# Optimization experiments

Measured on AMD Instinct MI355X. Metric: run time of the kernel, lower is better.

Reference implementation:

```python
import math
import jax, jax.numpy as jnp
import numpy as np

B, L, D, H, FF = 32, 796, 512, 8, 2048
HD = D // H          # 64
CS, STRIDE = 16, 13  # clip_size=16, overlap_area_size=3 -> stride 13
NC = (L - CS) // STRIDE + 1  # 61 clips, tiles L exactly


def _ln(v):
    m = jnp.mean(v, axis=-1, keepdims=True)
    s = jnp.mean((v - m) ** 2, axis=-1, keepdims=True)
    return (v - m) / jnp.sqrt(s + 1e-6)


def setup_inputs() -> dict:
    key = jax.random.key(0)
    ks = iter(jax.random.split(key, 64))
    def w(*shape):
        return jax.random.normal(next(ks), shape, jnp.float32) * 0.02
    inp = {
        "x": jax.random.normal(next(ks), (B, L, D), jnp.float32),
        "mask": jnp.ones((B, 1, L), dtype=bool),
        # global block params
        "g_ln_g": jnp.ones((D,), jnp.float32), "g_ln_b": jnp.zeros((D,), jnp.float32),
        "Wq": w(D, D), "Wk": w(D, D), "Wv": w(D, D), "Wo": w(D, D),
        "bq": jnp.zeros((D,), jnp.float32), "bk": jnp.zeros((D,), jnp.float32),
        "bv": jnp.zeros((D,), jnp.float32), "bo": jnp.zeros((D,), jnp.float32),
        "f_ln_g": jnp.ones((D,), jnp.float32), "f_ln_b": jnp.zeros((D,), jnp.float32),
        "W1": w(D, FF), "b1": jnp.zeros((FF,), jnp.float32),
        "W2": w(FF, D), "b2": jnp.zeros((D,), jnp.float32),
        # per-batch-element clip params (ModuleList of 32 -> stacked leading dim B)
        "c_ln_g": jnp.ones((B, D), jnp.float32), "c_ln_b": jnp.zeros((B, D), jnp.float32),
        "cWq": w(B, D, D), "cWk": w(B, D, D), "cWv": w(B, D, D), "cWo": w(B, D, D),
        "cbq": jnp.zeros((B, D), jnp.float32), "cbk": jnp.zeros((B, D), jnp.float32),
        "cbv": jnp.zeros((B, D), jnp.float32), "cbo": jnp.zeros((B, D), jnp.float32),
        "cf_ln_g": jnp.ones((B, D), jnp.float32), "cf_ln_b": jnp.zeros((B, D), jnp.float32),
        "cW1": w(B, D, FF), "cb1": jnp.zeros((B, FF), jnp.float32),
        "cW2": w(B, FF, D), "cb2": jnp.zeros((B, D), jnp.float32),
    }
    return inp


def reference(x, mask, g_ln_g, g_ln_b, Wq, Wk, Wv, Wo, bq, bk, bv, bo,
              f_ln_g, f_ln_b, W1, b1, W2, b2,
              c_ln_g, c_ln_b, cWq, cWk, cWv, cWo, cbq, cbk, cbv, cbo,
              cf_ln_g, cf_ln_b, cW1, cb1, cW2, cb2):
    # ---- clip partition: overlapping length-16 windows, stride 13 ----
    starts = np.arange(NC) * STRIDE
    idx = starts[:, None] + np.arange(CS)            # [NC, CS]
    clips = x[:, idx]                                 # [B, NC, CS, D]
    cmask = mask[:, 0][:, idx]                        # [B, NC, CS]
    # channel shuffle on last 384 dims: view(nc,16,24,16).permute(0,3,2,1)
    c1 = clips[..., :128]
    c2 = clips[..., 128:].reshape(B, NC, CS, 24, 16)
    c2 = jnp.transpose(c2, (0, 1, 4, 3, 2)).reshape(B, NC, CS, 384)
    clips = jnp.concatenate([c1, c2], axis=-1)        # [B, NC, CS, D]
    # ---- per-batch-element clip LN + MHA + FFN (distinct weights per b) ----
    cn = _ln(clips) * c_ln_g[:, None, None, :] + c_ln_b[:, None, None, :]
    q = (jnp.einsum('bncd,bde->bnce', cn, cWq) + cbq[:, None, None, :]).reshape(B, NC, CS, H, HD)
    k = (jnp.einsum('bncd,bde->bnce', cn, cWk) + cbk[:, None, None, :]).reshape(B, NC, CS, H, HD)
    v = (jnp.einsum('bncd,bde->bnce', cn, cWv) + cbv[:, None, None, :]).reshape(B, NC, CS, H, HD)
    q = q / math.sqrt(HD)
    sc = jnp.einsum('bnqhd,bnkhd->bnhqk', q, k)       # [B, NC, H, CS, CS]
    sc = jnp.where(cmask[:, :, None, None, :], sc, -jnp.inf)
    a = jax.nn.softmax(sc, axis=-1)
    ctx = jnp.einsum('bnhqk,bnkhd->bnqhd', a, v).reshape(B, NC, CS, D)
    mh = jnp.einsum('bncd,bde->bnce', ctx, cWo) + cbo[:, None, None, :]
    hcl = mh + clips                                  # dropout = identity (eval)
    fn = _ln(hcl) * cf_ln_g[:, None, None, :] + cf_ln_b[:, None, None, :]
    fmid = jax.nn.relu(jnp.einsum('bncd,bdf->bncf', fn, cW1) + cb1[:, None, None, :])
    clips_out = jnp.einsum('bncf,bfd->bncd', fmid, cW2) + cb2[:, None, None, :] + hcl
    p = np.arange(L)
    cidx = np.minimum(p // STRIDE, NC - 1)
    off = p - cidx * STRIDE
    x_rec = clips_out[:, cidx, off]                   # [B, L, D]
    # ---- global LN + MHA + residual + FFN ----
    xn = _ln(x_rec) * g_ln_g + g_ln_b
    q2 = (xn @ Wq + bq).reshape(B, L, H, HD) / math.sqrt(HD)
    k2 = (xn @ Wk + bk).reshape(B, L, H, HD)
    v2 = (xn @ Wv + bv).reshape(B, L, H, HD)
    sc2 = jnp.einsum('bqhd,bkhd->bhqk', q2, k2)
    sc2 = jnp.where(mask[:, None, :, :], sc2, -jnp.inf)
    ctx2 = jnp.einsum('bhqk,bkhd->bqhd', jax.nn.softmax(sc2, axis=-1), v2).reshape(B, L, D)
    h = ctx2 @ Wo + bo + x
    hn = _ln(h) * f_ln_g + f_ln_b
    o = jax.nn.relu(hn @ W1 + b1) @ W2 + b2 + h
    return o
```

## Files before the change

### kernel.cpp

```cpp
#include <hip/hip_runtime.h>

#define B_   32
#define L_   796
#define D_   512
#define H_   8
#define HD_  64
#define FF_  2048
#define CS_  16
#define STR_ 13
#define NC_  61
#define NQT_ 13
#define NQT2_ 7
#define MC_  976
#define QKVS 1536
#define QS   (0.125f * 1.44269504f)

typedef __attribute__((ext_vector_type(8))) short short8;
typedef __attribute__((ext_vector_type(4))) short short4v;
typedef __attribute__((ext_vector_type(4))) float f32x4;

__device__ __forceinline__ unsigned short f2bf(float x) {
    unsigned u = __float_as_uint(x);
    unsigned r = u + 0x7FFFu + ((u >> 16) & 1u);
    return (unsigned short)(r >> 16);
}
__device__ __forceinline__ float bf2f(unsigned short h) {
    return __uint_as_float(((unsigned)h) << 16);
}
__device__ __forceinline__ float ex2(float x) {
    return __builtin_amdgcn_exp2f(x);
}
__device__ __forceinline__ void gload16(const unsigned short* g, unsigned short* l) {
    __builtin_amdgcn_global_load_lds(
        (const __attribute__((address_space(1))) void*)g,
        (__attribute__((address_space(3))) void*)l, 16, 0, 0);
}

__global__ __launch_bounds__(256) void k_ln(const float* __restrict__ in,
                                            unsigned short* __restrict__ out,
                                            const float* __restrict__ gamma,
                                            const float* __restrict__ beta,
                                            int rows_per_batch, int gstride, int gather)
{
    __shared__ float red[8];
    long long row = blockIdx.x;
    int tid = threadIdx.x;
    int b;
    float v0, v1;
    if (gather == 2) {
        b = (int)(row / MC_);
        int rr = (int)(row % MC_);
        int n = rr >> 4, c = rr & 15;
        long long xb = (long long)b * L_ * D_;
        int d0 = tid, st0, sd0;
        if (d0 < 128) { st0 = n * STR_ + c; sd0 = d0; }
        else { int j = d0 - 128; st0 = n * STR_ + (j & 15); sd0 = 128 + ((j >> 4) << 4) + c; }
        v0 = in[xb + (long long)st0 * D_ + sd0];
        int j1 = tid + 128;
        int st1 = n * STR_ + (j1 & 15), sd1 = 128 + ((j1 >> 4) << 4) + c;
        v1 = in[xb + (long long)st1 * D_ + sd1];
    } else {
        long long srow = row;
        if (gather == 1) {
            int p = (int)(row % L_);
            b = (int)(row / L_);
            int ci = p / STR_; if (ci > NC_ - 1) ci = NC_ - 1;
            srow = ((long long)b * NC_ + ci) * CS_ + (p - ci * STR_);
        } else {
            b = (int)(row / rows_per_batch);
        }
        const float* xr = in + srow * D_;
        v0 = xr[tid]; v1 = xr[tid + 256];
    }
    float s = v0 + v1;
#pragma unroll
    for (int off = 1; off < 64; off <<= 1) s += __shfl_xor(s, off);
    if ((tid & 63) == 0) red[tid >> 6] = s;
    __syncthreads();
    float mean = (red[0] + red[1] + red[2] + red[3]) * (1.0f / 512.0f);
    float d0 = v0 - mean, d1 = v1 - mean;
    float vv = d0 * d0 + d1 * d1;
#pragma unroll
    for (int off = 1; off < 64; off <<= 1) vv += __shfl_xor(vv, off);
    if ((tid & 63) == 0) red[4 + (tid >> 6)] = vv;
    __syncthreads();
    float var = (red[4] + red[5] + red[6] + red[7]) * (1.0f / 512.0f);
    float rstd = rsqrtf(var + 1e-6f);
    const float* g  = gamma + (long long)b * gstride;
    const float* bt = beta  + (long long)b * gstride;
    unsigned short* o = out + row * D_;
    o[tid]       = f2bf(d0 * rstd * g[tid]       + bt[tid]);
    o[tid + 256] = f2bf(d1 * rstd * g[tid + 256] + bt[tid + 256]);
}

__global__ __launch_bounds__(256) void k_wt(const float* __restrict__ W,
                                            unsigned short* __restrict__ T,
                                            int rowStride, int tStride,
                                            long long sWb, long long sTb)
{
    __shared__ float t[32][33];
    int z = blockIdx.z;
    const float* Wz = W + (long long)z * sWb;
    unsigned short* Tz = T + (long long)z * sTb;
    int n0 = blockIdx.x << 5, k0 = blockIdx.y << 5;
    int tx = threadIdx.x & 31, ty = threadIdx.x >> 5;
#pragma unroll
    for (int i = 0; i < 4; i++) {
        int k = ty + (i << 3);
        t[k][tx] = Wz[(long long)(k0 + k) * rowStride + n0 + tx];
    }
    __syncthreads();
#pragma unroll
    for (int i = 0; i < 4; i++) {
        int n = ty + (i << 3);
        Tz[(long long)(n0 + n) * tStride + k0 + tx] = f2bf(t[tx][n]);
    }
}

__global__ __launch_bounds__(256) void k_wt_stack(const float* __restrict__ Wa,
                                                  const float* __restrict__ Wb,
                                                  const float* __restrict__ Wc,
                                                  const float* __restrict__ Wd,
                                                  unsigned short* __restrict__ T,
                                                  int nb, int ntens, long long sWb)
{
    __shared__ float t[32][33];
    int z = blockIdx.z;
    int tt = z / nb, b = z % nb;
    const float* Wz = (tt == 0 ? Wa : tt == 1 ? Wb : tt == 2 ? Wc : Wd)
                      + (long long)b * sWb;
    unsigned short* Tz = T + ((long long)b * ntens + tt) * (512 * 512);
    int n0 = blockIdx.x << 5, k0 = blockIdx.y << 5;
    int tx = threadIdx.x & 31, ty = threadIdx.x >> 5;
#pragma unroll
    for (int i = 0; i < 4; i++) {
        int k = ty + (i << 3);
        t[k][tx] = Wz[(long long)(k0 + k) * 512 + n0 + tx];
    }
    __syncthreads();
#pragma unroll
    for (int i = 0; i < 4; i++) {
        int n = ty + (i << 3);
        Tz[(long long)(n0 + n) * 512 + k0 + tx] = f2bf(t[tx][n]);
    }
}

__global__ __launch_bounds__(512) void k_gemm_mfma(
    const unsigned short* __restrict__ A, const unsigned short* __restrict__ WT,
    const float* __restrict__ b0p, const float* __restrict__ b1p,
    const float* __restrict__ b2p,
    const float* res, const float* __restrict__ xg, void* Cout,
    int M, int N, int K, int ldwk, int NX, int NYd, int mode,
    long long sAb, long long sWb, long long sBb, long long sRb, long long sCb,
    float alpha, float alpha1, int relu, int biasmode, int resmode, int outbf16)
{
    __shared__ unsigned short lds[16384];
    int tid = threadIdx.x;

    int bid = blockIdx.x;
    int xcd = bid & 7, inner = bid >> 3;
    int x = inner % NX, t = inner / NX;
    int y, z;
    if (mode == 0) { y = t % NYd; z = (t / NYd) * 8 + xcd; }
    else           { y = t * 8 + xcd; z = 0; }
    int row0 = y << 7, col0 = x << 7;
    if (row0 >= M) return;

    const unsigned short* Ab = A + z * sAb;
    const unsigned short* Wb = WT + z * sWb;

    int w = tid >> 6, lane = tid & 63;
    int wr = (w >> 2) << 6;
    int wc = (w & 3) << 5;
    int l15 = lane & 15, lg = lane >> 4;
    int lrow4 = lane >> 2, lslot = lane & 3;

    f32x4 acc[4][2];
#pragma unroll
    for (int i = 0; i < 4; i++)
#pragma unroll
        for (int j = 0; j < 2; j++) acc[i][j] = (f32x4)0.f;

    const int nt = K >> 5;
    int srow = (w << 4) + lrow4;
    int skey = (srow >> 1) & 3;

#pragma unroll
    for (int pt = 0; pt < 2; ++pt) {
        int k0 = pt << 5;
        unsigned short* sA = lds + (pt << 13);
        unsigned short* sW = sA + 4096;
        gload16(Ab + (long long)(row0 + srow) * K + k0 + ((lslot ^ skey) << 3),
                sA + ((w << 4) << 5));
        gload16(Wb + (long long)(col0 + srow) * ldwk + k0 + ((lslot ^ skey) << 3),
                sW + ((w << 4) << 5));
    }

    for (int kt = 0; kt < nt; ++kt) {
        if (kt + 1 < nt) asm volatile("s_waitcnt vmcnt(2)" ::: "memory");
        else             asm volatile("s_waitcnt vmcnt(0)" ::: "memory");
        __builtin_amdgcn_s_barrier();

        unsigned short* lA = lds + ((kt & 1) << 13);
        unsigned short* lW = lA + 4096;

        short8 af[4], bfr[2];
#pragma unroll
        for (int mf = 0; mf < 4; mf++) {
            int r = wr + (mf << 4) + l15;
            af[mf] = *(const short8*)(lA + (r << 5) + ((lg ^ ((r >> 1) & 3)) << 3));
        }
#pragma unroll
        for (int nf = 0; nf < 2; nf++) {
            int r = wc + (nf << 4) + l15;
            bfr[nf] = *(const short8*)(lW + (r << 5) + ((lg ^ ((r >> 1) & 3)) << 3));
        }

        asm volatile("s_waitcnt lgkmcnt(0)" ::: "memory");
        __builtin_amdgcn_s_barrier();

        if (kt + 2 < nt) {
            int k0 = (kt + 2) << 5;
            gload16(Ab + (long long)(row0 + srow) * K + k0 + ((lslot ^ skey) << 3),
                    lA + ((w << 4) << 5));
            gload16(Wb + (long long)(col0 + srow) * ldwk + k0 + ((lslot ^ skey) << 3),
                    lW + ((w << 4) << 5));
        }

        __builtin_amdgcn_s_setprio(1);
#pragma unroll
        for (int mf = 0; mf < 4; mf++)
#pragma unroll
            for (int nf = 0; nf < 2; nf++)
                acc[mf][nf] = __builtin_amdgcn_mfma_f32_16x16x32_bf16(
                    af[mf], bfr[nf], acc[mf][nf], 0, 0, 0);
        __builtin_amdgcn_s_setprio(0);
    }

#pragma unroll
    for (int mf = 0; mf < 4; mf++) {
#pragma unroll
        for (int reg = 0; reg < 4; reg++) {
            int gr = row0 + wr + (mf << 4) + (lg << 2) + reg;
            if (gr >= M) continue;
#pragma unroll
            for (int nf = 0; nf < 2; nf++) {
                int gc = col0 + wc + (nf << 4) + l15;
                float v = acc[mf][nf][reg];
                if (biasmode == 1) v += b0p[z * sBb + gc];
                else if (biasmode == 3) {
                    const float* bp = gc < 512 ? b0p : (gc < 1024 ? b1p : b2p);
                    v += bp[z * sBb + (gc & 511)];
                }
                v *= (gc < 512) ? alpha : alpha1;
                if (relu) v = fmaxf(v, 0.f);
                if (resmode == 1) {
                    v += res[z * sRb + (long long)gr * N + gc];
                } else if (resmode == 2) {
                    int n = gr >> 4, c = gr & 15;
                    int st, sd;
                    if (gc < 128) { st = n * STR_ + c; sd = gc; }
                    else {
                        int jj = gc - 128;
                        st = n * STR_ + (jj & 15);
                        sd = 128 + ((jj >> 4) << 4) + c;
                    }
                    v += xg[((long long)z * L_ + st) * D_ + sd];
                }
                long long co = z * sCb + (long long)gr * N + gc;
                if (outbf16) ((unsigned short*)Cout)[co] = f2bf(v);
                else         ((float*)Cout)[co] = v;
            }
        }
    }
}

__global__ __launch_bounds__(256) void k_clip_attn(const unsigned short* __restrict__ qkv,
                                                   unsigned short* __restrict__ ctx)
{
    __shared__ float qs[CS_][65], ks[CS_][65], vs[CS_][65], ps[CS_][17];
    int id = blockIdx.x;
    int h = id & (H_ - 1);
    int n = (id / H_) % NC_;
    int b = id / (H_ * NC_);
    long long base = (((long long)b * NC_ + n) * CS_) * QKVS + h * HD_;
    int tid = threadIdx.x;
    {
        int e = tid << 2;
        int r = e >> 6, c = e & 63;
        long long ro = base + (long long)r * QKVS + c;
        short4v qv = *(const short4v*)(qkv + ro);
        short4v kv = *(const short4v*)(qkv + ro + 512);
        short4v vv = *(const short4v*)(qkv + ro + 1024);
#pragma unroll
        for (int j = 0; j < 4; j++) {
            qs[r][c + j] = bf2f((unsigned short)qv[j]);
            ks[r][c + j] = bf2f((unsigned short)kv[j]);
            vs[r][c + j] = bf2f((unsigned short)vv[j]);
        }
    }
    __syncthreads();
    int qr = tid >> 4, kc = tid & 15;
    float s = 0.f;
#pragma unroll
    for (int d = 0; d < HD_; d++) s += qs[qr][d] * ks[kc][d];
    float m = s;
#pragma unroll
    for (int off = 1; off < 16; off <<= 1) m = fmaxf(m, __shfl_xor(m, off));
    float e = ex2(s - m);
    float sum = e;
#pragma unroll
    for (int off = 1; off < 16; off <<= 1) sum += __shfl_xor(sum, off);
    ps[qr][kc] = e / sum;
    __syncthreads();
    int dg = (tid & 15) * 4;
    float o0 = 0, o1 = 0, o2 = 0, o3 = 0;
#pragma unroll
    for (int kk = 0; kk < CS_; kk++) {
        float pp = ps[qr][kk];
        o0 += pp * vs[kk][dg + 0];
        o1 += pp * vs[kk][dg + 1];
        o2 += pp * vs[kk][dg + 2];
        o3 += pp * vs[kk][dg + 3];
    }
    long long ob = ((((long long)b * NC_ + n) * CS_) + qr) * D_ + h * HD_ + dg;
    short4v ov;
    ov[0] = (short)f2bf(o0); ov[1] = (short)f2bf(o1);
    ov[2] = (short)f2bf(o2); ov[3] = (short)f2bf(o3);
    *(short4v*)(ctx + ob) = ov;
}

__global__ __launch_bounds__(512) void k_flash_mfma(
    const unsigned short* __restrict__ qkv,
    unsigned short* __restrict__ out)
{
    __shared__ unsigned short sh[16384];
    unsigned short* lQ = sh;
    unsigned short* lK = sh + 8192;
    unsigned short* lV = sh + 12288;
    int bid = blockIdx.x;
    int h  = bid & 7;
    int inner = bid >> 3;
    int qt = inner % NQT2_;
    int b  = inner / NQT2_;
    int tid = threadIdx.x;
    int q0 = qt * 128;
    long long base = (long long)b * L_ * QKVS + h * HD_;

    int w = tid >> 6, lane = tid & 63;
    int l15 = lane & 15, lg = lane >> 4;
    int lrow = lane >> 3, lslot = lane & 7;
    int srow = lane;
    int sd0  = w << 3;

#pragma unroll
    for (int i = 0; i < 2; i++) {
        int cb = (w << 4) + (i << 3);
        int rr = cb + lrow;
        gload16(qkv + base + (long long)(q0 + rr) * QKVS + ((lslot ^ (rr & 7)) << 3),
                lQ + (cb << 6));
    }
    __syncthreads();

    int qrow = (w << 4) + l15;
    short8 qf[2];
#pragma unroll
    for (int ks = 0; ks < 2; ks++) {
        int slot = (ks << 2) + lg;
        qf[ks] = *(const short8*)(lQ + qrow * 64 + ((slot ^ (qrow & 7)) << 3));
    }
    asm volatile("s_waitcnt lgkmcnt(0)" ::: "memory");
    unsigned short* lPw = lQ + (w << 10);

    float m[4], l[4];
    f32x4 oacc[4];
#pragma unroll
    for (int r = 0; r < 4; r++) { m[r] = -1e30f; l[r] = 0.f; }
#pragma unroll
    for (int nf = 0; nf < 4; nf++) oacc[nf] = (f32x4)0.f;

    for (int kt = 0; kt < NQT_; kt++) {
        int k0 = kt * 64;
        __syncthreads();
        {
            int rr = (w << 3) + lrow;
            gload16(qkv + base + 512 + (long long)(k0 + rr) * QKVS + ((lslot ^ (rr & 7)) << 3),
                    lK + ((w << 3) << 6));
        }
        {
            int gr = k0 + srow;
            short8 v0 = (short8)0;
            if (gr < L_) {
                const unsigned short* pv = qkv + base + 1024 + (long long)gr * QKVS + sd0;
                v0 = *(const short8*)pv;
            }
            int ts = srow >> 3, t7 = srow & 7;
#pragma unroll
            for (int i = 0; i < 8; i++) {
                int d = sd0 + i;
                lV[d * 64 + ((ts ^ (d & 7)) << 3) + t7] = (unsigned short)v0[i];
            }
        }
        __syncthreads();

        f32x4 acc[4];
#pragma unroll
        for (int nf = 0; nf < 4; nf++) {
            acc[nf] = (f32x4)0.f;
            int tok = (nf << 4) + l15;
            int key = tok & 7;
#pragma unroll
            for (int ks = 0; ks < 2; ks++) {
                int slot = (ks << 2) + lg;
                short8 kf = *(const short8*)(lK + tok * 64 + ((slot ^ key) << 3));
                acc[nf] = __builtin_amdgcn_mfma_f32_16x16x32_bf16(qf[ks], kf, acc[nf], 0, 0, 0);
            }
        }
        if (kt == NQT_ - 1) {
#pragma unroll
            for (int nf = 0; nf < 4; nf++) {
                bool oob = (k0 + (nf << 4) + l15) >= L_;
#pragma unroll
                for (int r = 0; r < 4; r++)
                    if (oob) acc[nf][r] = -1e30f;
            }
        }
        float rm[4];
#pragma unroll
        for (int r = 0; r < 4; r++) rm[r] = -1e30f;
#pragma unroll
        for (int nf = 0; nf < 4; nf++) {
#pragma unroll
            for (int r = 0; r < 4; r++) rm[r] = fmaxf(rm[r], acc[nf][r]);
        }
#pragma unroll
        for (int off = 1; off < 16; off <<= 1) {
#pragma unroll
            for (int r = 0; r < 4; r++) rm[r] = fmaxf(rm[r], __shfl_xor(rm[r], off));
        }
        bool need = false;
#pragma unroll
        for (int r = 0; r < 4; r++) need = need || (rm[r] > m[r] + 8.0f);
        if (__ballot(need)) {
#pragma unroll
            for (int r = 0; r < 4; r++) {
                float mn = fmaxf(m[r], rm[r]);
                float sc = ex2(m[r] - mn);
                m[r] = mn;
                l[r] *= sc;
#pragma unroll
                for (int nf = 0; nf < 4; nf++) oacc[nf][r] *= sc;
            }
        }
        float ls[4];
#pragma unroll
        for (int r = 0; r < 4; r++) ls[r] = 0.f;
#pragma unroll
        for (int nf = 0; nf < 4; nf++) {
            int tok = (nf << 4) + l15;
            int slot = tok >> 3, t7 = tok & 7;
#pragma unroll
            for (int r = 0; r < 4; r++) {
                float p = ex2(acc[nf][r] - m[r]);
                ls[r] += p;
                int row = (lg << 2) + r;
                lPw[row * 64 + ((slot ^ (row & 7)) << 3) + t7] = f2bf(p);
            }
        }
#pragma unroll
        for (int off = 1; off < 16; off <<= 1) {
#pragma unroll
            for (int r = 0; r < 4; r++) ls[r] += __shfl_xor(ls[r], off);
        }
#pragma unroll
        for (int r = 0; r < 4; r++) l[r] += ls[r];
#pragma unroll
        for (int ks = 0; ks < 2; ks++) {
            int slot = (ks << 2) + lg;
            short8 pa = *(const short8*)(lPw + l15 * 64 + ((slot ^ (l15 & 7)) << 3));
#pragma unroll
            for (int nf = 0; nf < 4; nf++) {
                int d = (nf << 4) + l15;
                short8 vb = *(const short8*)(lV + d * 64 + ((slot ^ (d & 7)) << 3));
                oacc[nf] = __builtin_amdgcn_mfma_f32_16x16x32_bf16(pa, vb, oacc[nf], 0, 0, 0);
            }
        }
    }
    long long obase = (long long)b * L_ * D_ + h * HD_;
#pragma unroll
    for (int r = 0; r < 4; r++) {
        int gr = q0 + (w << 4) + (lg << 2) + r;
        if (gr >= L_) continue;
        float inv = 1.f / l[r];
        long long ob = obase + (long long)gr * D_;
#pragma unroll
        for (int nf = 0; nf < 4; nf++)
            out[ob + (nf << 4) + l15] = f2bf(oacc[nf][r] * inv);
    }
}

static inline void gemm(hipStream_t st, const unsigned short* A, const unsigned short* WTp,
                        const float* b0, const float* b1, const float* b2,
                        const float* res, const float* xg, void* C,
                        int M, int N, int K, int ldwk, int G,
                        long long sAb, long long sWb, long long sBb,
                        long long sRb, long long sCb,
                        float alpha, float alpha1, int relu, int biasmode,
                        int resmode, int outbf16)
{
    int NX = N / 128;
    int NY = (M + 127) >> 7;
    int mode = (G > 1) ? 0 : 1;
    int NYp = mode ? ((NY + 7) & ~7) : NY;
    int nblk = mode ? (NYp * NX) : (G * NY * NX);
    k_gemm_mfma<<<nblk, 512, 0, st>>>(A, WTp, b0, b1, b2, res, xg, C,
                                      M, N, K, ldwk, NX, NY, mode,
                                      sAb, sWb, sBb, sRb, sCb,
                                      alpha, alpha1, relu, biasmode, resmode, outbf16);
}

extern "C" void kernel_launch(void* const* d_in, const int* in_sizes, int n_in,
                              void* d_out, int out_size, void* d_ws, size_t ws_size,
                              hipStream_t stream)
{
    (void)in_sizes; (void)n_in; (void)out_size; (void)ws_size;
    const float* x      = (const float*)d_in[0];
    const float* g_ln_g = (const float*)d_in[2];
    const float* g_ln_b = (const float*)d_in[3];
    const float* Wq = (const float*)d_in[4];
    const float* Wk = (const float*)d_in[5];
    const float* Wv = (const float*)d_in[6];
    const float* Wo = (const float*)d_in[7];
    const float* bq = (const float*)d_in[8];
    const float* bk = (const float*)d_in[9];
    const float* bv = (const float*)d_in[10];
    const float* bo = (const float*)d_in[11];
    const float* f_ln_g = (const float*)d_in[12];
    const float* f_ln_b = (const float*)d_in[13];
    const float* W1 = (const float*)d_in[14];
    const float* b1 = (const float*)d_in[15];
    const float* W2 = (const float*)d_in[16];
    const float* b2 = (const float*)d_in[17];
    const float* c_ln_g = (const float*)d_in[18];
    const float* c_ln_b = (const float*)d_in[19];
    const float* cWq = (const float*)d_in[20];
    const float* cWk = (const float*)d_in[21];
    const float* cWv = (const float*)d_in[22];
    const float* cWo = (const float*)d_in[23];
    const float* cbq = (const float*)d_in[24];
    const float* cbk = (const float*)d_in[25];
    const float* cbv = (const float*)d_in[26];
    const float* cbo = (const float*)d_in[27];
    const float* cf_ln_g = (const float*)d_in[28];
    const float* cf_ln_b = (const float*)d_in[29];
    const float* cW1 = (const float*)d_in[30];
    const float* cb1 = (const float*)d_in[31];
    const float* cW2 = (const float*)d_in[32];
    const float* cb2 = (const float*)d_in[33];

    char* wsb = (char*)d_ws;
    float*          bA   = (float*)wsb;
    unsigned short* bB   = (unsigned short*)(wsb + (64ll  << 20));
    unsigned short* bQKV = (unsigned short*)(wsb + (96ll  << 20));
    unsigned short* wT   = (unsigned short*)(wsb + (188ll << 20));

    const long long sA   = (long long)MC_ * D_;
    const long long sQKV = (long long)MC_ * QKVS;
    const long long sWW  = (long long)D_ * D_;
    const int MG = B_ * L_;

    k_ln<<<B_ * MC_, 256, 0, stream>>>(x, bB, c_ln_g, c_ln_b, MC_, D_, 2);
    k_wt_stack<<<dim3(16, 16, 3 * B_), 256, 0, stream>>>(cWq, cWk, cWv, nullptr,
                                                         wT, B_, 3, sWW);
    gemm(stream, bB, wT, cbq, cbk, cbv, nullptr, nullptr, bQKV,
         MC_, QKVS, D_, D_, B_, sA, 3 * sWW, D_, 0, sQKV,
         QS, 1.0f, 0, 3, 0, 1);
    k_clip_attn<<<B_ * NC_ * H_, 256, 0, stream>>>(bQKV, bB);
    k_wt<<<dim3(16, 16, B_), 256, 0, stream>>>(cWo, wT, D_, D_, sWW, sWW);
    gemm(stream, bB, wT, cbo, nullptr, nullptr, nullptr, x, bA,
         MC_, D_, D_, D_, B_, sA, sWW, D_, 0, sA,
         1.0f, 1.0f, 0, 1, 2, 0);
    k_ln<<<B_ * MC_, 256, 0, stream>>>(bA, bB, cf_ln_g, cf_ln_b, MC_, D_, 0);
    for (int c = 0; c < 2; c++) {
        k_wt<<<dim3(32, 16, B_), 256, 0, stream>>>(cW1 + c * 1024, wT, FF_, D_,
                                                   (long long)D_ * FF_, 1024ll * D_);
        gemm(stream, bB, wT, cb1 + c * 1024, nullptr, nullptr, nullptr, nullptr, bQKV,
             MC_, 1024, D_, D_, B_, sA, 1024ll * D_, FF_, 0, (long long)MC_ * 1024,
             1.0f, 1.0f, 1, 1, 0, 1);
        k_wt<<<dim3(16, 32, B_), 256, 0, stream>>>(cW2 + (long long)c * 1024 * D_, wT,
                                                   D_, 1024, (long long)FF_ * D_,
                                                   (long long)D_ * 1024);
        gemm(stream, bQKV, wT, cb2, nullptr, nullptr, bA, nullptr, bA,
             MC_, D_, 1024, 1024, B_, (long long)MC_ * 1024, (long long)D_ * 1024,
             D_, sA, sA, 1.0f, 1.0f, 0, (c == 0) ? 1 : 0, 1, 0);
    }

    unsigned short* gQKVO = wT;
    unsigned short* gW1   = wT + 4 * 262144;
    unsigned short* gW2   = wT + 8 * 262144;
    k_wt_stack<<<dim3(16, 16, 4), 256, 0, stream>>>(Wq, Wk, Wv, Wo, gQKVO, 1, 4, 0);
    k_wt<<<dim3(64, 16, 1), 256, 0, stream>>>(W1, gW1, FF_, D_, 0, 0);
    k_wt<<<dim3(16, 64, 1), 256, 0, stream>>>(W2, gW2, D_, FF_, 0, 0);

    k_ln<<<MG, 256, 0, stream>>>(bA, bB, g_ln_g, g_ln_b, L_, 0, 1);
    gemm(stream, bB, gQKVO, bq, bk, bv, nullptr, nullptr, bQKV,
         MG, QKVS, D_, D_, 1, 0, 0, 0, 0, 0,
         QS, 1.0f, 0, 3, 0, 1);
    k_flash_mfma<<<B_ * H_ * NQT2_, 512, 0, stream>>>(bQKV, bB);
    gemm(stream, bB, gQKVO + 3 * 262144, bo, nullptr, nullptr, x, nullptr, bA,
         MG, D_, D_, D_, 1, 0, 0, 0, 0, 0,
         1.0f, 1.0f, 0, 1, 1, 0);
    k_ln<<<MG, 256, 0, stream>>>(bA, bB, f_ln_g, f_ln_b, MG, 0, 0);
    for (int c = 0; c < 2; c++) {
        gemm(stream, bB, gW1 + (long long)c * 1024 * 512, b1 + c * 1024,
             nullptr, nullptr, nullptr, nullptr, bQKV,
             MG, 1024, D_, D_, 1, 0, 0, 0, 0, 0,
             1.0f, 1.0f, 1, 1, 0, 1);
        gemm(stream, bQKV, gW2 + c * 1024, b2, nullptr, nullptr,
             (c == 0) ? bA : (float*)d_out, nullptr, d_out,
             MG, D_, 1024, FF_, 1, 0, 0, 0, 0, 0,
             1.0f, 1.0f, 0, (c == 0) ? 1 : 0, 1, 0);
    }
}
```

Measured before the change: 1.380 ms.

## Double-buffer K/V tiles in flash attention to overlap loads with compute

The global flash-attention kernel now keeps two LDS buffers for K and V. It issues the next tile's K load and V register load right after the QK^T MFMAs of the current tile, and removes one __syncthreads per iteration. This hides global-memory latency behind the softmax and PV compute. In exchange it uses more shared memory (48KB instead of 32KB), which may lower occupancy, and it holds the prefetched V fragment in registers.

Measured after the change: 1.377 ms. Within noise of the previous version (-0.3%).

```diff
diff --git a/kernel.cpp b/kernel.cpp
--- a/kernel.cpp
+++ b/kernel.cpp
@@ -334,10 +334,10 @@
     const unsigned short* __restrict__ qkv,
     unsigned short* __restrict__ out)
 {
-    __shared__ unsigned short sh[16384];
-    unsigned short* lQ = sh;
-    unsigned short* lK = sh + 8192;
-    unsigned short* lV = sh + 12288;
+    __shared__ unsigned short sh[24576];
+    unsigned short* lQ  = sh;
+    unsigned short* lKb = sh + 8192;
+    unsigned short* lVb = sh + 16384;
     int bid = blockIdx.x;
     int h  = bid & 7;
     int inner = bid >> 3;
@@ -360,6 +360,12 @@
         gload16(qkv + base + (long long)(q0 + rr) * QKVS + ((lslot ^ (rr & 7)) << 3),
                 lQ + (cb << 6));
     }
+    {
+        int rr = (w << 3) + lrow;
+        gload16(qkv + base + 512 + (long long)rr * QKVS + ((lslot ^ (rr & 7)) << 3),
+                lKb + ((w << 3) << 6));
+    }
+    short8 vreg = *(const short8*)(qkv + base + 1024 + (long long)srow * QKVS + sd0);
     __syncthreads();
 
     int qrow = (w << 4) + l15;
@@ -379,27 +385,15 @@
 #pragma unroll
     for (int nf = 0; nf < 4; nf++) oacc[nf] = (f32x4)0.f;
 
+    int ts = srow >> 3, t7 = srow & 7;
     for (int kt = 0; kt < NQT_; kt++) {
         int k0 = kt * 64;
-        __syncthreads();
-        {
-            int rr = (w << 3) + lrow;
-            gload16(qkv + base + 512 + (long long)(k0 + rr) * QKVS + ((lslot ^ (rr & 7)) << 3),
-                    lK + ((w << 3) << 6));
-        }
-        {
-            int gr = k0 + srow;
-            short8 v0 = (short8)0;
-            if (gr < L_) {
-                const unsigned short* pv = qkv + base + 1024 + (long long)gr * QKVS + sd0;
-                v0 = *(const short8*)pv;
-            }
-            int ts = srow >> 3, t7 = srow & 7;
-#pragma unroll
-            for (int i = 0; i < 8; i++) {
-                int d = sd0 + i;
-                lV[d * 64 + ((ts ^ (d & 7)) << 3) + t7] = (unsigned short)v0[i];
-            }
+        unsigned short* lK = lKb + ((kt & 1) << 12);
+        unsigned short* lV = lVb + ((kt & 1) << 12);
+#pragma unroll
+        for (int i = 0; i < 8; i++) {
+            int d = sd0 + i;
+            lV[d * 64 + ((ts ^ (d & 7)) << 3) + t7] = (unsigned short)vreg[i];
         }
         __syncthreads();
 
@@ -416,6 +410,16 @@
                 acc[nf] = __builtin_amdgcn_mfma_f32_16x16x32_bf16(qf[ks], kf, acc[nf], 0, 0, 0);
             }
         }
+        if (kt + 1 < NQT_) {
+            int k0n = (kt + 1) << 6;
+            int rr = (w << 3) + lrow;
+            gload16(qkv + base + 512 + (long long)(k0n + rr) * QKVS + ((lslot ^ (rr & 7)) << 3),
+                    lKb + (((kt + 1) & 1) << 12) + ((w << 3) << 6));
+            int grn = k0n + srow;
+            vreg = (short8)0;
+            if (grn < L_)
+                vreg = *(const short8*)(qkv + base + 1024 + (long long)grn * QKVS + sd0);
+        }
         if (kt == NQT_ - 1) {
 #pragma unroll
             for (int nf = 0; nf < 4; nf++) {
@@ -458,13 +462,13 @@
 #pragma unroll
         for (int nf = 0; nf < 4; nf++) {
             int tok = (nf << 4) + l15;
-            int slot = tok >> 3, t7 = tok & 7;
+            int slot = tok >> 3, tt7 = tok & 7;
 #pragma unroll
             for (int r = 0; r < 4; r++) {
                 float p = ex2(acc[nf][r] - m[r]);
                 ls[r] += p;
                 int row = (lg << 2) + r;
-                lPw[row * 64 + ((slot ^ (row & 7)) << 3) + t7] = f2bf(p);
+                lPw[row * 64 + ((slot ^ (row & 7)) << 3) + tt7] = f2bf(p);
             }
         }
 #pragma unroll
```
